# Optimization experiments

Measured on AMD Instinct MI355X. Metric: run time of the kernel, lower is better.

Reference implementation:

```python
import jax, jax.numpy as jnp
import numpy as np

DECAY = 0.99
EPSILON = 1e-05
N_TOKENS = 32768
EMBED_DIM = 256
NUM_EMB = 4096


def setup_inputs() -> dict:
    key = jax.random.key(0)
    k1, k2, k3 = jax.random.split(key, 3)
    return {
        "inputs": jax.random.normal(k1, (N_TOKENS, EMBED_DIM), dtype=jnp.float32),
        "codebook": jax.random.normal(k2, (NUM_EMB, EMBED_DIM), dtype=jnp.float32),
        "ema_w": jax.random.normal(k3, (NUM_EMB, EMBED_DIM), dtype=jnp.float32),
        "ema_cluster_size": jnp.zeros((NUM_EMB,), dtype=jnp.float32),
    }


def reference(inputs, codebook, ema_w, ema_cluster_size):
    K, D = codebook.shape
    flat = inputs.reshape(-1, D)  # [N, D]
    distances = (
        jnp.sum(flat * flat, axis=1, keepdims=True)
        + jnp.sum(codebook * codebook, axis=1)
        - 2.0 * flat @ codebook.T
    )
    encoding_indices = jnp.argmin(distances, axis=1)  # [N]
    encodings = jax.nn.one_hot(encoding_indices, K, dtype=flat.dtype)  # [N, K]
    quantized = codebook[encoding_indices].reshape(inputs.shape)  # [N, D]

    # EMA update (training branch). dw = encodings.T @ flat expressed as a
    # segment sum to avoid a second [N,K]-sized contraction pass.
    dw = jax.ops.segment_sum(flat, encoding_indices, num_segments=K)  # [K, D]
    counts = jax.ops.segment_sum(
        jnp.ones((flat.shape[0],), dtype=flat.dtype), encoding_indices, num_segments=K
    )  # [K]
    new_ema_w = ema_w * DECAY + (1.0 - DECAY) * dw
    cs = ema_cluster_size * DECAY + (1.0 - DECAY) * counts
    n = jnp.sum(cs)
    cs = (cs + EPSILON) / (n + K * EPSILON) * n  # laplace smoothing
    new_codebook = new_ema_w / cs[:, None]
    return quantized, encodings, new_codebook, new_ema_w, cs
```

## Files before the change

kernel.cpp:

```cpp
#include <hip/hip_runtime.h>
#include <hip/hip_bf16.h>

#define NTOK 32768
#define KEMB 4096
#define DDIM 256
#define DECAYF 0.99f
#define EPSF 1e-5f
#define KSPLIT 256
#define FLAG_THETA 0.11f
#define PRUNE_MARGIN 0.28f
#define SBIAS 4096.0f

#define B_AHAT  0ull
#define B_BHAT  16777216ull
#define B_PART  18874368ull
#define B_CE    52428800ull
#define B_CNTI  52445184ull
#define B_CSP   52461568ull
#define B_OFFS  52477952ull
#define B_NPTR  52494336ull
#define B_TIDX  52494400ull
#define B_TLIST 52887616ull
#define B_DW    53018688ull

#define OFF_Q  0ull
#define OFF_E  8388608ull
#define OFF_CB 142606336ull
#define OFF_W  143654912ull
#define OFF_CS 144703488ull

typedef __attribute__((ext_vector_type(8))) _Float16 f16x8;
typedef __attribute__((ext_vector_type(4))) _Float16 f16x4;
typedef __attribute__((ext_vector_type(4))) float f32x4;

__global__ __launch_bounds__(256) void prep_kernel(const float* __restrict__ xg,
                                                   const float* __restrict__ cbg,
                                                   _Float16* __restrict__ Ahat,
                                                   _Float16* __restrict__ Bhat,
                                                   float* __restrict__ ce,
                                                   int* __restrict__ countsI,
                                                   float4* __restrict__ dwv) {
    int b = blockIdx.x;
    int tid = threadIdx.x;
    if (b < 4096) {
        size_t gid = (size_t)b * 256 + tid;
        const float* sp = xg + gid * 8;
        f16x8 v;
        #pragma unroll
        for (int t = 0; t < 8; ++t) v[t] = (_Float16)sp[t];
        *(f16x8*)(Ahat + gid * 8) = v;
    } else if (b < 5120) {
        int k = (b - 4096) * 4 + (tid >> 6);
        int lane = tid & 63;
        float4 v = *(const float4*)(cbg + (size_t)k * DDIM + lane * 4);
        f16x4 h;
        h[0] = (_Float16)v.x; h[1] = (_Float16)v.y;
        h[2] = (_Float16)v.z; h[3] = (_Float16)v.w;
        *(f16x4*)(Bhat + (size_t)k * DDIM + lane * 4) = h;
        float s = v.x * v.x + v.y * v.y + v.z * v.z + v.w * v.w;
        #pragma unroll
        for (int o = 32; o > 0; o >>= 1) s += __shfl_down(s, o);
        if (lane == 0) ce[k] = s;
    } else if (b < 5136) {
        countsI[(b - 5120) * 256 + tid] = 0;
    } else {
        float4 z = {0.f, 0.f, 0.f, 0.f};
        dwv[(size_t)(b - 5136) * 256 + tid] = z;
    }
}

__global__ __launch_bounds__(256) void gemm_argmin_kernel(
        const _Float16* __restrict__ Ahat,
        const _Float16* __restrict__ Bhat,
        const float* __restrict__ ceg,
        float2* __restrict__ part) {
    __shared__ _Float16 As[128 * 64];
    __shared__ _Float16 Bs[128 * 64];
    const int tid  = threadIdx.x;
    const int lane = tid & 63;
    const int wave = tid >> 6;
    const int wm = wave >> 1, wn = wave & 1;

    int lin = blockIdx.y * 32 + blockIdx.x;
    lin = (lin & 7) * 1024 + (lin >> 3);
    const int nb = lin & 31, mb = lin >> 5;

    const int col = lane & 15, q = lane >> 4;
    const int cswz = q ^ (col & 7);

    const int srow = tid >> 3;
    const int sswz = (tid & 7) ^ (srow & 7);
    const _Float16* ag = Ahat + (size_t)(mb * 128 + srow) * KSPLIT + sswz * 8;
    const _Float16* bg = Bhat + (size_t)(nb * 128 + srow) * KSPLIT + sswz * 8;

    f32x4 zero = {0.f, 0.f, 0.f, 0.f};
    f32x4 acc[4][4];
    #pragma unroll
    for (int i = 0; i < 4; ++i)
        #pragma unroll
        for (int j = 0; j < 4; ++j) acc[i][j] = zero;

    for (int kt = 0; kt < KSPLIT / 64; ++kt) {
        __syncthreads();
        #pragma unroll
        for (int n = 0; n < 4; ++n) {
            __builtin_amdgcn_global_load_lds(
                (const __attribute__((address_space(1))) void*)(ag + (size_t)n * 32 * KSPLIT + kt * 64),
                (__attribute__((address_space(3))) void*)(As + n * 2048 + tid * 8), 16, 0, 0);
            __builtin_amdgcn_global_load_lds(
                (const __attribute__((address_space(1))) void*)(bg + (size_t)n * 32 * KSPLIT + kt * 64),
                (__attribute__((address_space(3))) void*)(Bs + n * 2048 + tid * 8), 16, 0, 0);
        }
        __syncthreads();

        const f16x8* Av = (const f16x8*)As;
        const f16x8* Bv = (const f16x8*)Bs;
        #pragma unroll
        for (int ks = 0; ks < 2; ++ks) {
            f16x8 a[4], b[4];
            #pragma unroll
            for (int i = 0; i < 4; ++i)
                a[i] = Av[(wm * 64 + i * 16 + col) * 8 + (cswz ^ (ks * 4))];
            #pragma unroll
            for (int j = 0; j < 4; ++j)
                b[j] = Bv[(wn * 64 + j * 16 + col) * 8 + (cswz ^ (ks * 4))];
            #pragma unroll
            for (int i = 0; i < 4; ++i)
                #pragma unroll
                for (int j = 0; j < 4; ++j)
                    acc[i][j] = __builtin_amdgcn_mfma_f32_16x16x32_f16(a[i], b[j], acc[i][j], 0, 0, 0);
        }
    }

    float ce_j[4];
    #pragma unroll
    for (int j = 0; j < 4; ++j) ce_j[j] = ceg[nb * 128 + wn * 64 + j * 16 + col];

    #pragma unroll
    for (int i = 0; i < 4; ++i) {
        #pragma unroll
        for (int r = 0; r < 4; ++r) {
            float p1 = 3.4e38f, p2 = 3.4e38f;
            #pragma unroll
            for (int j = 0; j < 4; ++j) {
                float s = ce_j[j] - 2.0f * acc[i][j][r] + SBIAS;
                int loc = j * 16 + col;
                float sp = __int_as_float((__float_as_int(s) & ~63) | loc);
                if (sp < p1) { p2 = p1; p1 = sp; }
                else if (sp < p2) { p2 = sp; }
            }
            #pragma unroll
            for (int m = 1; m < 16; m <<= 1) {
                float o1 = __shfl_xor(p1, m, 16);
                float o2 = __shfl_xor(p2, m, 16);
                float lo = fminf(p1, o1);
                float hi = fmaxf(p1, o1);
                p2 = fminf(hi, fminf(p2, o2));
                p1 = lo;
            }
            if (col == i * 4 + r) {
                int mrow = mb * 128 + wm * 64 + i * 16 + q * 4 + r;
                float2 p;
                p.x = p1; p.y = p2;
                part[(size_t)mrow * 64 + nb * 2 + wn] = p;
            }
        }
    }
}

__global__ __launch_bounds__(256) void post_kernel(const float* __restrict__ xg,
                                                   const float* __restrict__ cb,
                                                   const float2* __restrict__ part,
                                                   int* __restrict__ tokIdx,
                                                   int* __restrict__ countsI,
                                                   float* __restrict__ quant,
                                                   float* __restrict__ enc) {
    int row = blockIdx.x * 4 + (threadIdx.x >> 6);
    int lane = threadIdx.x & 63;
    float2 p = part[(size_t)row * 64 + lane];
    float own = p.x;
    float b1 = p.x, b2 = p.y;
    #pragma unroll
    for (int m = 1; m < 64; m <<= 1) {
        float o1 = __shfl_xor(b1, m);
        float o2 = __shfl_xor(b2, m);
        float lo = fminf(b1, o1);
        float hi = fmaxf(b1, o1);
        b2 = fminf(hi, fminf(b2, o2));
        b1 = lo;
    }
    int kfin;
    {
        unsigned long long wmask = __ballot(own == b1);
        int wl = __ffsll(wmask) - 1;
        kfin = wl * 64 + (__float_as_int(b1) & 63);
    }
    if (b2 - b1 < FLAG_THETA) {
        unsigned long long mask = __ballot(own <= b1 + PRUNE_MARGIN);
        double best = 1e300;
        int bi = 0x7fffffff;
        const float* xr = xg + (size_t)row * DDIM;
        while (mask) {
            int c = __ffsll(mask) - 1;
            mask &= mask - 1;
            int k = c * 64 + lane;
            const float* e = cb + (size_t)k * DDIM;
            double s = 0.0;
            for (int d4 = 0; d4 < DDIM / 4; ++d4) {
                float4 e4 = *(const float4*)(e + d4 * 4);
                float4 x4 = *(const float4*)(xr + d4 * 4);
                double e0 = (double)e4.x, e1 = (double)e4.y;
                double e2 = (double)e4.z, e3 = (double)e4.w;
                s += e0 * (e0 - 2.0 * (double)x4.x) + e1 * (e1 - 2.0 * (double)x4.y)
                   + e2 * (e2 - 2.0 * (double)x4.z) + e3 * (e3 - 2.0 * (double)x4.w);
            }
            if (s < best || (s == best && k < bi)) { best = s; bi = k; }
        }
        #pragma unroll
        for (int m = 1; m < 64; m <<= 1) {
            double ob = __shfl_xor(best, m);
            int   oi  = __shfl_xor(bi, m);
            if (ob < best || (ob == best && oi < bi)) { best = ob; bi = oi; }
        }
        kfin = bi;
    }
    if (lane == 0) {
        tokIdx[row] = kfin;
        atomicAdd(countsI + kfin, 1);
    }
    {
        float4* er = (float4*)(enc + (size_t)row * KEMB);
        int kf4 = kfin >> 2, kc = kfin & 3;
        #pragma unroll
        for (int v = 0; v < 16; ++v) {
            int f4 = v * 64 + lane;
            float4 val = {0.f, 0.f, 0.f, 0.f};
            if (f4 == kf4) ((float*)&val)[kc] = 1.0f;
            er[f4] = val;
        }
    }
    float4 e = *(const float4*)(cb + (size_t)kfin * DDIM + lane * 4);
    *(float4*)(quant + (size_t)row * DDIM + lane * 4) = e;
}

__global__ __launch_bounds__(256) void scan_cs_kernel(const int* __restrict__ countsI,
                                                      const float* __restrict__ ema_cs,
                                                      int* __restrict__ offs,
                                                      float* __restrict__ cs_pre,
                                                      float* __restrict__ nptr) {
    __shared__ int part[256];
    __shared__ float npart[256];
    __shared__ int pref[257];
    int tid = threadIdx.x;
    int local[16];
    int s = 0;
    float ns = 0.0f;
    #pragma unroll
    for (int i = 0; i < 16; ++i) {
        int c = countsI[tid * 16 + i];
        local[i] = c;
        s += c;
        float csp = ema_cs[tid * 16 + i] * DECAYF + (1.0f - DECAYF) * (float)c;
        cs_pre[tid * 16 + i] = csp;
        ns += csp;
    }
    part[tid] = s;
    npart[tid] = ns;
    __syncthreads();
    if (tid == 0) {
        pref[0] = 0;
        float nn = 0.0f;
        for (int i = 0; i < 256; ++i) {
            pref[i + 1] = pref[i] + part[i];
            nn += npart[i];
        }
        nptr[0] = nn;
    }
    __syncthreads();
    int run = pref[tid];
    #pragma unroll
    for (int i = 0; i < 16; ++i) { offs[tid * 16 + i] = run; run += local[i]; }
}

__global__ __launch_bounds__(256) void filllist_kernel(const int* __restrict__ tokIdx,
                                                       int* __restrict__ offs,
                                                       int* __restrict__ tlist) {
    int t = blockIdx.x * 256 + threadIdx.x;
    int k = tokIdx[t];
    int slot = atomicAdd(offs + k, 1);
    tlist[slot] = t;
}

#define SEG_CHUNK 32
__global__ __launch_bounds__(256) void segdw_kernel(const float* __restrict__ xg,
                                                    const int* __restrict__ tlist,
                                                    const int* __restrict__ tokIdx,
                                                    float* __restrict__ dw) {
    int tid = threadIdx.x;
    int s0 = blockIdx.x * SEG_CHUNK;
    float acc = 0.0f;
    int curk = -1;
    for (int s = s0; s < s0 + SEG_CHUNK; ++s) {
        int t = tlist[s];
        int k = tokIdx[t];
        if (k != curk) {
            if (curk >= 0) atomicAdd(dw + (size_t)curk * DDIM + tid, acc);
            acc = 0.0f;
            curk = k;
        }
        acc += xg[(size_t)t * DDIM + tid];
    }
    if (curk >= 0) atomicAdd(dw + (size_t)curk * DDIM + tid, acc);
}

__global__ __launch_bounds__(256) void epi_kernel(const float* __restrict__ ema_w,
                                                  const float* __restrict__ dw,
                                                  const float* __restrict__ cs_pre,
                                                  const float* __restrict__ nptr,
                                                  float* __restrict__ new_cb,
                                                  float* __restrict__ new_w,
                                                  float* __restrict__ cs_out) {
    int gid = blockIdx.x * 256 + threadIdx.x;
    int k = gid >> 8, d = gid & 255;
    float n = *nptr;
    float csp = cs_pre[k];
    float cs = (csp + EPSF) / (n + (float)KEMB * EPSF) * n;
    float w = ema_w[gid] * DECAYF + (1.0f - DECAYF) * dw[gid];
    new_w[gid] = w;
    new_cb[gid] = w / cs;
    if (d == 0) cs_out[k] = cs;
}

extern "C" void kernel_launch(void* const* d_in, const int* in_sizes, int n_in,
                              void* d_out, int out_size, void* d_ws, size_t ws_size,
                              hipStream_t stream) {
    const float* xg     = (const float*)d_in[0];
    const float* cbg    = (const float*)d_in[1];
    const float* ema_w  = (const float*)d_in[2];
    const float* ema_cs = (const float*)d_in[3];

    float* out = (float*)d_out;
    unsigned char* wsb = (unsigned char*)d_ws;

    float* quant  = out + OFF_Q;
    float* enc    = out + OFF_E;
    float* new_cb = out + OFF_CB;
    float* new_w  = out + OFF_W;
    float* cs_out = out + OFF_CS;

    _Float16* Ahat = (_Float16*)(wsb + B_AHAT);
    _Float16* Bhat = (_Float16*)(wsb + B_BHAT);
    float2* part   = (float2*)(wsb + B_PART);
    float* ce      = (float*)(wsb + B_CE);
    int*   countsI = (int*)(wsb + B_CNTI);
    float* cs_pre  = (float*)(wsb + B_CSP);
    int*   offs    = (int*)(wsb + B_OFFS);
    float* nptr    = (float*)(wsb + B_NPTR);
    int*   tokIdx  = (int*)(wsb + B_TIDX);
    int*   tlist   = (int*)(wsb + B_TLIST);
    float* dw      = (float*)(wsb + B_DW);

    prep_kernel<<<6160, 256, 0, stream>>>(xg, cbg, Ahat, Bhat, ce, countsI, (float4*)dw);
    gemm_argmin_kernel<<<dim3(KEMB / 128, NTOK / 128), 256, 0, stream>>>(Ahat, Bhat, ce, part);
    post_kernel<<<NTOK / 4, 256, 0, stream>>>(xg, cbg, part, tokIdx, countsI, quant, enc);
    scan_cs_kernel<<<1, 256, 0, stream>>>(countsI, ema_cs, offs, cs_pre, nptr);
    filllist_kernel<<<NTOK / 256, 256, 0, stream>>>(tokIdx, offs, tlist);
    segdw_kernel<<<NTOK / SEG_CHUNK, 256, 0, stream>>>(xg, tlist, tokIdx, dw);
    epi_kernel<<<(KEMB * DDIM) / 256, 256, 0, stream>>>(ema_w, dw, cs_pre, nptr,
                                                        new_cb, new_w, cs_out);
}
```

Baseline: 797.5 us.

## Fuse post-processing into GEMM via last-block-per-row-tile counter

Removes the separate post kernel. Each GEMM block bumps a per-row-tile atomic counter, and the last of the 32 column blocks for a row tile does the argmin finalisation, fp64 refinement, one-hot and quantized writes for its 128 rows. This saves a kernel launch and lets the post work overlap with other GEMM blocks. In exchange, the tail work lands on only 256 blocks doing 32 rows each, which lowers parallelism for the encoding writes of about 134MB. The added threadfence and atomics cost little.

New measurement: 1.900 ms. +138.3%, slower.

```diff
diff --git a/kernel.cpp b/kernel.cpp
--- a/kernel.cpp
+++ b/kernel.cpp
@@ -22,6 +22,7 @@
 #define B_TIDX  52494400ull
 #define B_TLIST 52887616ull
 #define B_DW    53018688ull
+#define B_CTR   57212992ull
 
 #define OFF_Q  0ull
 #define OFF_E  8388608ull
@@ -39,7 +40,8 @@
                                                    _Float16* __restrict__ Bhat,
                                                    float* __restrict__ ce,
                                                    int* __restrict__ countsI,
-                                                   float4* __restrict__ dwv) {
+                                                   float4* __restrict__ dwv,
+                                                   int* __restrict__ ctr) {
     int b = blockIdx.x;
     int tid = threadIdx.x;
     if (b < 4096) {
@@ -63,17 +65,26 @@
         if (lane == 0) ce[k] = s;
     } else if (b < 5136) {
         countsI[(b - 5120) * 256 + tid] = 0;
-    } else {
+    } else if (b < 6160) {
         float4 z = {0.f, 0.f, 0.f, 0.f};
         dwv[(size_t)(b - 5136) * 256 + tid] = z;
-    }
-}
-
-__global__ __launch_bounds__(256) void gemm_argmin_kernel(
+    } else {
+        ctr[tid] = 0;
+    }
+}
+
+__global__ __launch_bounds__(256) void gemm_fused_kernel(
         const _Float16* __restrict__ Ahat,
         const _Float16* __restrict__ Bhat,
         const float* __restrict__ ceg,
-        float2* __restrict__ part) {
+        float2* __restrict__ part,
+        const float* __restrict__ xg,
+        const float* __restrict__ cb,
+        int* __restrict__ tokIdx,
+        int* __restrict__ countsI,
+        int* __restrict__ ctr,
+        float* __restrict__ quant,
+        float* __restrict__ enc) {
     __shared__ _Float16 As[128 * 64];
     __shared__ _Float16 Bs[128 * 64];
     const int tid  = threadIdx.x;
@@ -166,81 +177,81 @@
             }
         }
     }
-}
-
-__global__ __launch_bounds__(256) void post_kernel(const float* __restrict__ xg,
-                                                   const float* __restrict__ cb,
-                                                   const float2* __restrict__ part,
-                                                   int* __restrict__ tokIdx,
-                                                   int* __restrict__ countsI,
-                                                   float* __restrict__ quant,
-                                                   float* __restrict__ enc) {
-    int row = blockIdx.x * 4 + (threadIdx.x >> 6);
-    int lane = threadIdx.x & 63;
-    float2 p = part[(size_t)row * 64 + lane];
-    float own = p.x;
-    float b1 = p.x, b2 = p.y;
-    #pragma unroll
-    for (int m = 1; m < 64; m <<= 1) {
-        float o1 = __shfl_xor(b1, m);
-        float o2 = __shfl_xor(b2, m);
-        float lo = fminf(b1, o1);
-        float hi = fmaxf(b1, o1);
-        b2 = fminf(hi, fminf(b2, o2));
-        b1 = lo;
-    }
-    int kfin;
-    {
-        unsigned long long wmask = __ballot(own == b1);
-        int wl = __ffsll(wmask) - 1;
-        kfin = wl * 64 + (__float_as_int(b1) & 63);
-    }
-    if (b2 - b1 < FLAG_THETA) {
-        unsigned long long mask = __ballot(own <= b1 + PRUNE_MARGIN);
-        double best = 1e300;
-        int bi = 0x7fffffff;
-        const float* xr = xg + (size_t)row * DDIM;
-        while (mask) {
-            int c = __ffsll(mask) - 1;
-            mask &= mask - 1;
-            int k = c * 64 + lane;
-            const float* e = cb + (size_t)k * DDIM;
-            double s = 0.0;
-            for (int d4 = 0; d4 < DDIM / 4; ++d4) {
-                float4 e4 = *(const float4*)(e + d4 * 4);
-                float4 x4 = *(const float4*)(xr + d4 * 4);
-                double e0 = (double)e4.x, e1 = (double)e4.y;
-                double e2 = (double)e4.z, e3 = (double)e4.w;
-                s += e0 * (e0 - 2.0 * (double)x4.x) + e1 * (e1 - 2.0 * (double)x4.y)
-                   + e2 * (e2 - 2.0 * (double)x4.z) + e3 * (e3 - 2.0 * (double)x4.w);
-            }
-            if (s < best || (s == best && k < bi)) { best = s; bi = k; }
-        }
+
+    __threadfence();
+    __shared__ int lastS;
+    if (tid == 0) lastS = (atomicAdd(ctr + mb, 1) == 31);
+    __syncthreads();
+    if (!lastS) return;
+    __threadfence();
+
+    for (int it = 0; it < 32; ++it) {
+        int row = mb * 128 + (wave << 5) + it;
+        float2 pp = part[(size_t)row * 64 + lane];
+        float own = pp.x;
+        float b1 = pp.x, b2 = pp.y;
         #pragma unroll
         for (int m = 1; m < 64; m <<= 1) {
-            double ob = __shfl_xor(best, m);
-            int   oi  = __shfl_xor(bi, m);
-            if (ob < best || (ob == best && oi < bi)) { best = ob; bi = oi; }
-        }
-        kfin = bi;
-    }
-    if (lane == 0) {
-        tokIdx[row] = kfin;
-        atomicAdd(countsI + kfin, 1);
-    }
-    {
-        float4* er = (float4*)(enc + (size_t)row * KEMB);
-        int kf4 = kfin >> 2, kc = kfin & 3;
-        #pragma unroll
-        for (int v = 0; v < 16; ++v) {
-            int f4 = v * 64 + lane;
-            float4 val = {0.f, 0.f, 0.f, 0.f};
-            if (f4 == kf4) ((float*)&val)[kc] = 1.0f;
-            er[f4] = val;
-        }
-    }
-    float4 e = *(const float4*)(cb + (size_t)kfin * DDIM + lane * 4);
-    *(float4*)(quant + (size_t)row * DDIM + lane * 4) = e;
+            float o1 = __shfl_xor(b1, m);
+            float o2 = __shfl_xor(b2, m);
+            float lo = fminf(b1, o1);
+            float hi = fmaxf(b1, o1);
+            b2 = fminf(hi, fminf(b2, o2));
+            b1 = lo;
+        }
+        int kfin;
+        {
+            unsigned long long wmask = __ballot(own == b1);
+            int wl = __ffsll(wmask) - 1;
+            kfin = wl * 64 + (__float_as_int(b1) & 63);
+        }
+        if (b2 - b1 < FLAG_THETA) {
+            unsigned long long mask = __ballot(own <= b1 + PRUNE_MARGIN);
+            double best = 1e300;
+            int bi = 0x7fffffff;
+            const float* xr = xg + (size_t)row * DDIM;
+            while (mask) {
+                int c = __ffsll(mask) - 1;
+                mask &= mask - 1;
+                int k = c * 64 + lane;
+                const float* e = cb + (size_t)k * DDIM;
+                double s = 0.0;
+                for (int d4 = 0; d4 < DDIM / 4; ++d4) {
+                    float4 e4 = *(const float4*)(e + d4 * 4);
+                    float4 x4 = *(const float4*)(xr + d4 * 4);
+                    double e0 = (double)e4.x, e1 = (double)e4.y;
+                    double e2 = (double)e4.z, e3 = (double)e4.w;
+                    s += e0 * (e0 - 2.0 * (double)x4.x) + e1 * (e1 - 2.0 * (double)x4.y)
+                       + e2 * (e2 - 2.0 * (double)x4.z) + e3 * (e3 - 2.0 * (double)x4.w);
+                }
+                if (s < best || (s == best && k < bi)) { best = s; bi = k; }
+            }
+            #pragma unroll
+            for (int m = 1; m < 64; m <<= 1) {
+                double ob = __shfl_xor(best, m);
+                int   oi  = __shfl_xor(bi, m);
+                if (ob < best || (ob == best && oi < bi)) { best = ob; bi = oi; }
+            }
+            kfin = bi;
+        }
+        if (lane == 0) {
+            tokIdx[row] = kfin;
+            atomicAdd(countsI + kfin, 1);
+        }
+        {
+            float4* er = (float4*)(enc + (size_t)row * KEMB);
+            int kf4 = kfin >> 2, kc = kfin & 3;
+            #pragma unroll
+            for (int v = 0; v < 16; ++v) {
+                int f4 = v * 64 + lane;
+                float4 val = {0.f, 0.f, 0.f, 0.f};
+                if (f4 == kf4) ((float*)&val)[kc] = 1.0f;
+                er[f4] = val;
+            }
+        }
+        float4 e = *(const float4*)(cb + (size_t)kfin * DDIM + lane * 4);
+        *(float4*)(quant + (size_t)row * DDIM + lane * 4) = e;
+    }
 }
 
 __global__ __launch_bounds__(256) void scan_cs_kernel(const int* __restrict__ countsI,
@@ -359,10 +370,12 @@
     int*   tokIdx  = (int*)(wsb + B_TIDX);
     int*   tlist   = (int*)(wsb + B_TLIST);
     float* dw      = (float*)(wsb + B_DW);
-
-    prep_kernel<<<6160, 256, 0, stream>>>(xg, cbg, Ahat, Bhat, ce, countsI, (float4*)dw);
-    gemm_argmin_kernel<<<dim3(KEMB / 128, NTOK / 128), 256, 0, stream>>>(Ahat, Bhat, ce, part);
-    post_kernel<<<NTOK / 4, 256, 0, stream>>>(xg, cbg, part, tokIdx, countsI, quant, enc);
+    int*   ctr     = (int*)(wsb + B_CTR);
+
+    prep_kernel<<<6161, 256, 0, stream>>>(xg, cbg, Ahat, Bhat, ce, countsI,
+                                          (float4*)dw, ctr);
+    gemm_fused_kernel<<<dim3(KEMB / 128, NTOK / 128), 256, 0, stream>>>(
+        Ahat, Bhat, ce, part, xg, cbg, tokIdx, countsI, ctr, quant, enc);
     scan_cs_kernel<<<1, 256, 0, stream>>>(countsI, ema_cs, offs, cs_pre, nptr);
     filllist_kernel<<<NTOK / 256, 256, 0, stream>>>(tokIdx, offs, tlist);
     segdw_kernel<<<NTOK / SEG_CHUNK, 256, 0, stream>>>(xg, tlist, tokIdx, dw);
```
